# Kernel optimization log

Measured on AMD Instinct MI355X. Metric: run time of the kernel, lower is better.

The kernel has to match this reference:

```python
import jax, jax.numpy as jnp
import numpy as np

L, B, S, D, H, F = 8, 8, 2048, 1024, 16, 4096
DH = D // H
EPS = 1e-5


def setup_inputs() -> dict:
    key = jax.random.key(0)
    ks = jax.random.split(key, 8)
    sc = 0.02
    return {
        "x": jax.random.normal(ks[0], (B, S, D), jnp.float32),
        "layer_indices": jax.random.randint(ks[1], (B,), 0, L, jnp.int32),
        "Wq": jax.random.normal(ks[2], (L, D, D), jnp.float32) * sc,
        "bq": jnp.zeros((L, D), jnp.float32),
        "Wk": jax.random.normal(ks[3], (L, D, D), jnp.float32) * sc,
        "bk": jnp.zeros((L, D), jnp.float32),
        "Wv": jax.random.normal(ks[4], (L, D, D), jnp.float32) * sc,
        "bv": jnp.zeros((L, D), jnp.float32),
        "Wo": jax.random.normal(ks[5], (L, D, D), jnp.float32) * sc,
        "bo": jnp.zeros((L, D), jnp.float32),
        "ln1_s": jnp.ones((L, D), jnp.float32),
        "ln1_b": jnp.zeros((L, D), jnp.float32),
        "ln2_s": jnp.ones((L, D), jnp.float32),
        "ln2_b": jnp.zeros((L, D), jnp.float32),
        "W1": jax.random.normal(ks[6], (L, D, F), jnp.float32) * sc,
        "b1": jnp.zeros((L, F), jnp.float32),
        "W2": jax.random.normal(ks[7], (L, F, D), jnp.float32) * sc,
        "b2": jnp.zeros((L, D), jnp.float32),
    }


def _layernorm(x, s, b):
    # x: [B,S,D]; s,b: [B,D] (per-routed-layer params)
    m = jnp.mean(x, axis=-1, keepdims=True)
    v = jnp.mean(jnp.square(x - m), axis=-1, keepdims=True)
    return (x - m) * jax.lax.rsqrt(v + EPS) * s[:, None, :] + b[:, None, :]


def reference(x, layer_indices, Wq, bq, Wk, bk, Wv, bv, Wo, bo,
              ln1_s, ln1_b, ln2_s, ln2_b, W1, b1, W2, b2):
    idx = layer_indices
    # Gather each batch element's routed layer parameters (MoE-style dispatch).
    Wq_g, bq_g = Wq[idx], bq[idx]
    Wk_g, bk_g = Wk[idx], bk[idx]
    Wv_g, bv_g = Wv[idx], bv[idx]
    Wo_g, bo_g = Wo[idx], bo[idx]
    s1, b1n = ln1_s[idx], ln1_b[idx]
    s2, b2n = ln2_s[idx], ln2_b[idx]
    W1_g, bf1 = W1[idx], b1[idx]
    W2_g, bf2 = W2[idx], b2[idx]

    # --- Multi-head self-attention (pre-LN) ---
    h = _layernorm(x, s1, b1n)                                   # [B,S,D]
    q = jnp.einsum('bsd,bde->bse', h, Wq_g) + bq_g[:, None, :]
    k = jnp.einsum('bsd,bde->bse', h, Wk_g) + bk_g[:, None, :]
    v = jnp.einsum('bsd,bde->bse', h, Wv_g) + bv_g[:, None, :]
    q = q.reshape(B, S, H, DH)
    k = k.reshape(B, S, H, DH)
    v = v.reshape(B, S, H, DH)
    scores = jnp.einsum('bqhd,bkhd->bhqk', q, k) / np.sqrt(DH)   # [B,H,S,S]
    probs = jax.nn.softmax(scores, axis=-1)
    attn = jnp.einsum('bhqk,bkhd->bqhd', probs, v).reshape(B, S, D)
    attn = jnp.einsum('bsd,bde->bse', attn, Wo_g) + bo_g[:, None, :]
    x = x + attn

    # --- Feed-forward (pre-LN) ---
    h = _layernorm(x, s2, b2n)
    h = jax.nn.gelu(jnp.einsum('bsd,bdf->bsf', h, W1_g) + bf1[:, None, :])
    h = jnp.einsum('bsf,bfd->bsd', h, W2_g) + bf2[:, None, :]
    return x + h
```

## Files before the change

### kernel.cpp

```cpp
#include <hip/hip_runtime.h>
#include <cstdint>
#include <cstddef>

typedef __attribute__((ext_vector_type(8))) short s8v;
typedef __attribute__((ext_vector_type(4))) float f4v;

constexpr int Lc = 8, Bc = 8, Sc = 2048, Dc = 1024, Hc = 16, Fc = 4096;

__device__ __forceinline__ unsigned short f2bf(float f) {
    unsigned int u = __float_as_uint(f);
    u = (u + 0x7FFFu + ((u >> 16) & 1u)) >> 16;
    return (unsigned short)u;
}

__global__ __launch_bounds__(256) void transpose_cast(
    const float* __restrict__ in, unsigned short* __restrict__ out, int R, int C) {
    __shared__ float tile[32][33];
    int l = blockIdx.z;
    int r0 = blockIdx.y << 5, c0 = blockIdx.x << 5;
    const float* ip = in + (size_t)l * R * C;
    unsigned short* op = out + (size_t)l * R * C;
    int tx = threadIdx.x & 31, ty = threadIdx.x >> 5;
#pragma unroll
    for (int i = 0; i < 4; i++)
        tile[ty + i * 8][tx] = ip[(size_t)(r0 + ty + i * 8) * C + (c0 + tx)];
    __syncthreads();
#pragma unroll
    for (int i = 0; i < 4; i++)
        op[(size_t)(c0 + ty + i * 8) * R + (r0 + tx)] = f2bf(tile[tx][ty + i * 8]);
}

__global__ __launch_bounds__(256) void ln_kernel(
    const float* __restrict__ x, const float* __restrict__ sc, const float* __restrict__ bi,
    const int* __restrict__ idx, unsigned short* __restrict__ out) {
    int row = blockIdx.x;
    int b = row >> 11;
    int l = idx[b];
    const float* xr = x + (size_t)row * Dc;
    int t = threadIdx.x;
    float4 xv = *(const float4*)(xr + t * 4);
    float s = xv.x + xv.y + xv.z + xv.w;
    float ss = xv.x * xv.x + xv.y * xv.y + xv.z * xv.z + xv.w * xv.w;
#pragma unroll
    for (int off = 32; off; off >>= 1) { s += __shfl_xor(s, off); ss += __shfl_xor(ss, off); }
    __shared__ float red[2][4];
    int w = t >> 6, lane = t & 63;
    if (lane == 0) { red[0][w] = s; red[1][w] = ss; }
    __syncthreads();
    float tot = red[0][0] + red[0][1] + red[0][2] + red[0][3];
    float tots = red[1][0] + red[1][1] + red[1][2] + red[1][3];
    float mean = tot * (1.0f / Dc);
    float var = tots * (1.0f / Dc) - mean * mean;
    float r = rsqrtf(var + 1e-5f);
    float4 s4 = *(const float4*)(sc + (size_t)l * Dc + t * 4);
    float4 b4 = *(const float4*)(bi + (size_t)l * Dc + t * 4);
    ushort4 o;
    o.x = f2bf((xv.x - mean) * r * s4.x + b4.x);
    o.y = f2bf((xv.y - mean) * r * s4.y + b4.y);
    o.z = f2bf((xv.z - mean) * r * s4.z + b4.z);
    o.w = f2bf((xv.w - mean) * r * s4.w + b4.w);
    *(ushort4*)(out + (size_t)row * Dc + t * 4) = o;
}

template <int EPI>
__global__ __launch_bounds__(256) void gemm_kernel(
    const unsigned short* __restrict__ A, const unsigned short* __restrict__ Wt,
    const float* __restrict__ bias, const int* __restrict__ idx,
    const float* __restrict__ resid, void* __restrict__ out, int M, int N, int K) {
    int b = blockIdx.z;
    int l = idx[b];
    int m0 = blockIdx.y << 7, n0 = blockIdx.x << 7;
    const unsigned short* Ab = A + (size_t)b * M * K;
    const unsigned short* Wl = Wt + (size_t)l * N * K;
    __shared__ alignas(16) unsigned short As[128][40];
    __shared__ alignas(16) unsigned short Bs[128][40];
    int tid = threadIdx.x, w = tid >> 6, lane = tid & 63, quad = lane >> 4, lr = lane & 15;
    int wm = (w >> 1) << 6, wn = (w & 1) << 6;
    f4v acc[4][4];
#pragma unroll
    for (int i = 0; i < 4; i++)
#pragma unroll
        for (int j = 0; j < 4; j++) acc[i][j] = 0.f;

    int srow = tid >> 1, soff = (tid & 1) * 16;
    const unsigned short* ag = Ab + (size_t)(m0 + srow) * K + soff;
    const unsigned short* bg = Wl + (size_t)(n0 + srow) * K + soff;

    for (int k0 = 0; k0 < K; k0 += 32) {
        uint4 av0 = *(const uint4*)(ag + k0);
        uint4 av1 = *(const uint4*)(ag + k0 + 8);
        uint4 bv0 = *(const uint4*)(bg + k0);
        uint4 bv1 = *(const uint4*)(bg + k0 + 8);
        __syncthreads();
        *(uint4*)&As[srow][soff] = av0;
        *(uint4*)&As[srow][soff + 8] = av1;
        *(uint4*)&Bs[srow][soff] = bv0;
        *(uint4*)&Bs[srow][soff + 8] = bv1;
        __syncthreads();
        s8v af[4], bf[4];
#pragma unroll
        for (int i = 0; i < 4; i++) af[i] = *(const s8v*)&As[wm + i * 16 + lr][quad * 8];
#pragma unroll
        for (int j = 0; j < 4; j++) bf[j] = *(const s8v*)&Bs[wn + j * 16 + lr][quad * 8];
#pragma unroll
        for (int i = 0; i < 4; i++)
#pragma unroll
            for (int j = 0; j < 4; j++)
                acc[i][j] = __builtin_amdgcn_mfma_f32_16x16x32_bf16(af[i], bf[j], acc[i][j], 0, 0, 0);
    }

    float bj[4];
#pragma unroll
    for (int j = 0; j < 4; j++) bj[j] = bias[(size_t)l * N + (n0 + wn + j * 16 + lr)];
    size_t obase = (size_t)b * M * N;
#pragma unroll
    for (int i = 0; i < 4; i++) {
#pragma unroll
        for (int r = 0; r < 4; r++) {
            int gm = m0 + wm + i * 16 + quad * 4 + r;
            size_t rowoff = obase + (size_t)gm * N;
#pragma unroll
            for (int j = 0; j < 4; j++) {
                int gn = n0 + wn + j * 16 + lr;
                float val = acc[i][j][r] + bj[j];
                if constexpr (EPI == 0) {
                    ((unsigned short*)out)[rowoff + gn] = f2bf(val);
                } else if constexpr (EPI == 1) {
                    float g = 0.5f * val * (1.0f + tanhf(0.7978845608f * (val + 0.044715f * val * val * val)));
                    ((unsigned short*)out)[rowoff + gn] = f2bf(g);
                } else {
                    ((float*)out)[rowoff + gn] = resid[rowoff + gn] + val;
                }
            }
        }
    }
}

__global__ __launch_bounds__(256) void flash_kernel(
    const unsigned short* __restrict__ qm, const unsigned short* __restrict__ km,
    const unsigned short* __restrict__ vm, unsigned short* __restrict__ om) {
    const int b = blockIdx.z, h = blockIdx.y, q0 = blockIdx.x << 6;
    const int tid = threadIdx.x, w = tid >> 6, lane = tid & 63, quad = lane >> 4, lr = lane & 15;
    __shared__ alignas(16) unsigned short Pl[4][16][72];
    __shared__ alignas(16) unsigned short Vt[64][72];
    const size_t bS = (size_t)b * Sc;
    const int hoff = h << 6;

    s8v aq0, aq1;
    {
        const unsigned short* qr = qm + (bS + q0 + w * 16 + lr) * (size_t)Dc + hoff;
        aq0 = *(const s8v*)(qr + quad * 8);
        aq1 = *(const s8v*)(qr + 32 + quad * 8);
    }
    f4v accO[4];
#pragma unroll
    for (int i = 0; i < 4; i++) accO[i] = 0.f;
    float m_i[4] = {-3e38f, -3e38f, -3e38f, -3e38f};
    float l_i[4] = {0.f, 0.f, 0.f, 0.f};

    const int vkey = tid >> 2, vc = tid & 3;

    for (int kv0 = 0; kv0 < Sc; kv0 += 64) {
        const unsigned short* vp = vm + (bS + kv0 + vkey) * (size_t)Dc + hoff + vc * 16;
        s8v v0 = *(const s8v*)vp;
        s8v v1 = *(const s8v*)(vp + 8);
        __syncthreads();
#pragma unroll
        for (int e = 0; e < 8; e++) {
            Vt[vc * 16 + e][vkey] = (unsigned short)v0[e];
            Vt[vc * 16 + 8 + e][vkey] = (unsigned short)v1[e];
        }
        f4v sc4[4];
#pragma unroll
        for (int j = 0; j < 4; j++) {
            const unsigned short* kr = km + (bS + kv0 + j * 16 + lr) * (size_t)Dc + hoff;
            s8v b0 = *(const s8v*)(kr + quad * 8);
            s8v b1 = *(const s8v*)(kr + 32 + quad * 8);
            f4v c = 0.f;
            c = __builtin_amdgcn_mfma_f32_16x16x32_bf16(aq0, b0, c, 0, 0, 0);
            c = __builtin_amdgcn_mfma_f32_16x16x32_bf16(aq1, b1, c, 0, 0, 0);
            sc4[j] = c * 0.125f;
        }
        float alpha[4], pmat[4][4];
#pragma unroll
        for (int rr = 0; rr < 4; rr++) {
            float lm = fmaxf(fmaxf(sc4[0][rr], sc4[1][rr]), fmaxf(sc4[2][rr], sc4[3][rr]));
#pragma unroll
            for (int off = 1; off < 16; off <<= 1) lm = fmaxf(lm, __shfl_xor(lm, off));
            float mn = fmaxf(m_i[rr], lm);
            alpha[rr] = __expf(m_i[rr] - mn);
            m_i[rr] = mn;
            float ls = 0.f;
#pragma unroll
            for (int j = 0; j < 4; j++) {
                float p = __expf(sc4[j][rr] - mn);
                pmat[j][rr] = p;
                ls += p;
            }
#pragma unroll
            for (int off = 1; off < 16; off <<= 1) ls += __shfl_xor(ls, off);
            l_i[rr] = l_i[rr] * alpha[rr] + ls;
        }
#pragma unroll
        for (int jd = 0; jd < 4; jd++)
#pragma unroll
            for (int rr = 0; rr < 4; rr++) accO[jd][rr] *= alpha[rr];
#pragma unroll
        for (int j = 0; j < 4; j++)
#pragma unroll
            for (int rr = 0; rr < 4; rr++)
                Pl[w][quad * 4 + rr][j * 16 + lr] = f2bf(pmat[j][rr]);
        __syncthreads();
        s8v ap0 = *(const s8v*)&Pl[w][lr][quad * 8];
        s8v ap1 = *(const s8v*)&Pl[w][lr][32 + quad * 8];
#pragma unroll
        for (int jd = 0; jd < 4; jd++) {
            s8v b0 = *(const s8v*)&Vt[jd * 16 + lr][quad * 8];
            s8v b1 = *(const s8v*)&Vt[jd * 16 + lr][32 + quad * 8];
            accO[jd] = __builtin_amdgcn_mfma_f32_16x16x32_bf16(ap0, b0, accO[jd], 0, 0, 0);
            accO[jd] = __builtin_amdgcn_mfma_f32_16x16x32_bf16(ap1, b1, accO[jd], 0, 0, 0);
        }
    }
#pragma unroll
    for (int jd = 0; jd < 4; jd++)
#pragma unroll
        for (int rr = 0; rr < 4; rr++)
            om[(bS + q0 + w * 16 + quad * 4 + rr) * (size_t)Dc + hoff + jd * 16 + lr] =
                f2bf(accO[jd][rr] / l_i[rr]);
}

extern "C" void kernel_launch(void* const* d_in, const int* in_sizes, int n_in,
                              void* d_out, int out_size, void* d_ws, size_t ws_size,
                              hipStream_t stream) {
    const float* x  = (const float*)d_in[0];
    const int* idx  = (const int*)d_in[1];
    const float* Wq = (const float*)d_in[2];  const float* bq  = (const float*)d_in[3];
    const float* Wk = (const float*)d_in[4];  const float* bk  = (const float*)d_in[5];
    const float* Wv = (const float*)d_in[6];  const float* bv  = (const float*)d_in[7];
    const float* Wo = (const float*)d_in[8];  const float* bo  = (const float*)d_in[9];
    const float* s1 = (const float*)d_in[10]; const float* b1n = (const float*)d_in[11];
    const float* s2 = (const float*)d_in[12]; const float* b2n = (const float*)d_in[13];
    const float* W1 = (const float*)d_in[14]; const float* bf1 = (const float*)d_in[15];
    const float* W2 = (const float*)d_in[16]; const float* bf2 = (const float*)d_in[17];

    const size_t eDD  = (size_t)Lc * Dc * Dc;
    const size_t eDF  = (size_t)Lc * Dc * Fc;
    const size_t eBSD = (size_t)Bc * Sc * Dc;
    unsigned short* Wtq = (unsigned short*)d_ws;
    unsigned short* Wtk = Wtq + eDD;
    unsigned short* Wtv = Wtk + eDD;
    unsigned short* Wto = Wtv + eDD;
    unsigned short* Wt1 = Wto + eDD;
    unsigned short* Wt2 = Wt1 + eDF;
    unsigned short* hb  = Wt2 + eDF;
    unsigned short* qb  = hb + eBSD;
    unsigned short* kb  = qb + eBSD;
    unsigned short* vb  = kb + eBSD;
    unsigned short* ab  = vb + eBSD;
    float* x2           = (float*)(ab + eBSD);
    unsigned short* fb  = qb;

    dim3 blk(256);
    transpose_cast<<<dim3(Dc / 32, Dc / 32, Lc), blk, 0, stream>>>(Wq, Wtq, Dc, Dc);
    transpose_cast<<<dim3(Dc / 32, Dc / 32, Lc), blk, 0, stream>>>(Wk, Wtk, Dc, Dc);
    transpose_cast<<<dim3(Dc / 32, Dc / 32, Lc), blk, 0, stream>>>(Wv, Wtv, Dc, Dc);
    transpose_cast<<<dim3(Dc / 32, Dc / 32, Lc), blk, 0, stream>>>(Wo, Wto, Dc, Dc);
    transpose_cast<<<dim3(Fc / 32, Dc / 32, Lc), blk, 0, stream>>>(W1, Wt1, Dc, Fc);
    transpose_cast<<<dim3(Dc / 32, Fc / 32, Lc), blk, 0, stream>>>(W2, Wt2, Fc, Dc);
    ln_kernel<<<Bc * Sc, blk, 0, stream>>>(x, s1, b1n, idx, hb);
    gemm_kernel<0><<<dim3(Dc / 128, Sc / 128, Bc), blk, 0, stream>>>(hb, Wtq, bq, idx, nullptr, qb, Sc, Dc, Dc);
    gemm_kernel<0><<<dim3(Dc / 128, Sc / 128, Bc), blk, 0, stream>>>(hb, Wtk, bk, idx, nullptr, kb, Sc, Dc, Dc);
    gemm_kernel<0><<<dim3(Dc / 128, Sc / 128, Bc), blk, 0, stream>>>(hb, Wtv, bv, idx, nullptr, vb, Sc, Dc, Dc);
    flash_kernel<<<dim3(Sc / 64, Hc, Bc), blk, 0, stream>>>(qb, kb, vb, ab);
    gemm_kernel<2><<<dim3(Dc / 128, Sc / 128, Bc), blk, 0, stream>>>(ab, Wto, bo, idx, x, x2, Sc, Dc, Dc);
    ln_kernel<<<Bc * Sc, blk, 0, stream>>>(x2, s2, b2n, idx, hb);
    gemm_kernel<1><<<dim3(Fc / 128, Sc / 128, Bc), blk, 0, stream>>>(hb, Wt1, bf1, idx, nullptr, fb, Sc, Fc, Dc);
    gemm_kernel<2><<<dim3(Dc / 128, Sc / 128, Bc), blk, 0, stream>>>(fb, Wt2, bf2, idx, x2, (float*)d_out, Sc, Dc, Fc);
}
```

Before: 1.845 ms.

## Use direct global-to-LDS loads with swizzle in GEMM and register-only flash attention

The GEMM now stages tiles with global_load_lds into an unpadded LDS layout and applies an XOR swizzle to avoid bank conflicts, which removes the register round-trip. The flash kernel computes S^T so that the probabilities stay in registers as the MFMA B operand, which removes the LDS transposes of P and V. It reads V from a new pre-transposed buffer produced by a separate transpose_v kernel, and it stages the output through LDS so the final stores are coalesced. In exchange there is an extra transpose launch, and flash now reads K and V directly from global memory with no LDS reuse across waves.

After: 2.148 ms. 1.16x slower.

```diff
diff --git a/kernel.cpp b/kernel.cpp
--- a/kernel.cpp
+++ b/kernel.cpp
@@ -11,6 +11,12 @@
     unsigned int u = __float_as_uint(f);
     u = (u + 0x7FFFu + ((u >> 16) & 1u)) >> 16;
     return (unsigned short)u;
+}
+
+__device__ __forceinline__ void gload16(const unsigned short* g, unsigned short* l) {
+    __builtin_amdgcn_global_load_lds(
+        (const __attribute__((address_space(1))) unsigned int*)g,
+        (__attribute__((address_space(3))) unsigned int*)l, 16, 0, 0);
 }
 
 __global__ __launch_bounds__(256) void transpose_cast(
@@ -28,6 +34,23 @@
 #pragma unroll
     for (int i = 0; i < 4; i++)
         op[(size_t)(c0 + ty + i * 8) * R + (r0 + tx)] = f2bf(tile[tx][ty + i * 8]);
+}
+
+__global__ __launch_bounds__(256) void transpose_v(
+    const unsigned short* __restrict__ in, unsigned short* __restrict__ out) {
+    __shared__ unsigned short t[32][33];
+    int bh = blockIdx.z, b = bh >> 4, h = bh & 15;
+    int s0 = blockIdx.x << 5, d0 = blockIdx.y << 5;
+    int tx = threadIdx.x & 31, ty = threadIdx.x >> 5;
+    const unsigned short* ip = in + (size_t)(b * Sc + s0) * Dc + (h << 6) + d0;
+#pragma unroll
+    for (int i = 0; i < 4; i++)
+        t[ty + i * 8][tx] = ip[(size_t)(ty + i * 8) * Dc + tx];
+    __syncthreads();
+    unsigned short* op = out + ((size_t)(b * Hc + h) * 64 + d0) * Sc + s0;
+#pragma unroll
+    for (int i = 0; i < 4; i++)
+        op[(size_t)(ty + i * 8) * Sc + tx] = t[tx][ty + i * 8];
 }
 
 __global__ __launch_bounds__(256) void ln_kernel(
@@ -72,8 +95,8 @@
     int m0 = blockIdx.y << 7, n0 = blockIdx.x << 7;
     const unsigned short* Ab = A + (size_t)b * M * K;
     const unsigned short* Wl = Wt + (size_t)l * N * K;
-    __shared__ alignas(16) unsigned short As[128][40];
-    __shared__ alignas(16) unsigned short Bs[128][40];
+    __shared__ alignas(16) unsigned short As[128 * 32];
+    __shared__ alignas(16) unsigned short Bs[128 * 32];
     int tid = threadIdx.x, w = tid >> 6, lane = tid & 63, quad = lane >> 4, lr = lane & 15;
     int wm = (w >> 1) << 6, wn = (w & 1) << 6;
     f4v acc[4][4];
@@ -82,26 +105,30 @@
 #pragma unroll
         for (int j = 0; j < 4; j++) acc[i][j] = 0.f;
 
-    int srow = tid >> 1, soff = (tid & 1) * 16;
-    const unsigned short* ag = Ab + (size_t)(m0 + srow) * K + soff;
-    const unsigned short* bg = Wl + (size_t)(n0 + srow) * K + soff;
+    int srow = (w << 4) + (lane >> 2);
+    int schunk = (lane & 3) ^ ((lane >> 2) & 3);
+    const unsigned short* ag0 = Ab + (size_t)(m0 + srow) * K + (schunk << 3);
+    const unsigned short* ag1 = Ab + (size_t)(m0 + 64 + srow) * K + (schunk << 3);
+    const unsigned short* bg0 = Wl + (size_t)(n0 + srow) * K + (schunk << 3);
+    const unsigned short* bg1 = Wl + (size_t)(n0 + 64 + srow) * K + (schunk << 3);
+    unsigned short* la0 = As + ((w << 4) << 5);
+    unsigned short* la1 = As + ((64 + (w << 4)) << 5);
+    unsigned short* lb0 = Bs + ((w << 4) << 5);
+    unsigned short* lb1 = Bs + ((64 + (w << 4)) << 5);
+    int fchunk = (quad ^ (lr & 3)) << 3;
 
     for (int k0 = 0; k0 < K; k0 += 32) {
-        uint4 av0 = *(const uint4*)(ag + k0);
-        uint4 av1 = *(const uint4*)(ag + k0 + 8);
-        uint4 bv0 = *(const uint4*)(bg + k0);
-        uint4 bv1 = *(const uint4*)(bg + k0 + 8);
         __syncthreads();
-        *(uint4*)&As[srow][soff] = av0;
-        *(uint4*)&As[srow][soff + 8] = av1;
-        *(uint4*)&Bs[srow][soff] = bv0;
-        *(uint4*)&Bs[srow][soff + 8] = bv1;
+        gload16(ag0 + k0, la0);
+        gload16(ag1 + k0, la1);
+        gload16(bg0 + k0, lb0);
+        gload16(bg1 + k0, lb1);
         __syncthreads();
         s8v af[4], bf[4];
 #pragma unroll
-        for (int i = 0; i < 4; i++) af[i] = *(const s8v*)&As[wm + i * 16 + lr][quad * 8];
-#pragma unroll
-        for (int j = 0; j < 4; j++) bf[j] = *(const s8v*)&Bs[wn + j * 16 + lr][quad * 8];
+        for (int i = 0; i < 4; i++) af[i] = *(const s8v*)&As[((wm + i * 16 + lr) << 5) + fchunk];
+#pragma unroll
+        for (int j = 0; j < 4; j++) bf[j] = *(const s8v*)&Bs[((wn + j * 16 + lr) << 5) + fchunk];
 #pragma unroll
         for (int i = 0; i < 4; i++)
 #pragma unroll
@@ -138,95 +165,94 @@
 
 __global__ __launch_bounds__(256) void flash_kernel(
     const unsigned short* __restrict__ qm, const unsigned short* __restrict__ km,
-    const unsigned short* __restrict__ vm, unsigned short* __restrict__ om) {
+    const unsigned short* __restrict__ vT, unsigned short* __restrict__ om) {
     const int b = blockIdx.z, h = blockIdx.y, q0 = blockIdx.x << 6;
     const int tid = threadIdx.x, w = tid >> 6, lane = tid & 63, quad = lane >> 4, lr = lane & 15;
-    __shared__ alignas(16) unsigned short Pl[4][16][72];
-    __shared__ alignas(16) unsigned short Vt[64][72];
     const size_t bS = (size_t)b * Sc;
     const int hoff = h << 6;
 
-    s8v aq0, aq1;
-    {
-        const unsigned short* qr = qm + (bS + q0 + w * 16 + lr) * (size_t)Dc + hoff;
-        aq0 = *(const s8v*)(qr + quad * 8);
-        aq1 = *(const s8v*)(qr + 32 + quad * 8);
-    }
+    const unsigned short* qr = qm + (bS + q0 + (w << 4) + lr) * (size_t)Dc + hoff + (quad << 3);
+    s8v bq0 = *(const s8v*)qr;
+    s8v bq1 = *(const s8v*)(qr + 32);
+    const int krow_off = ((lr >> 2) << 3) + (lr & 3);
+    const unsigned short* kbase = km + bS * (size_t)Dc + hoff + (quad << 3);
+    const unsigned short* vbase = vT + ((size_t)(b * Hc + h) * 64 + lr) * Sc + (quad << 3);
+
     f4v accO[4];
 #pragma unroll
-    for (int i = 0; i < 4; i++) accO[i] = 0.f;
-    float m_i[4] = {-3e38f, -3e38f, -3e38f, -3e38f};
-    float l_i[4] = {0.f, 0.f, 0.f, 0.f};
-
-    const int vkey = tid >> 2, vc = tid & 3;
+    for (int d = 0; d < 4; d++) accO[d] = 0.f;
+    float m_s = -3e38f, l_s = 0.f;
 
     for (int kv0 = 0; kv0 < Sc; kv0 += 64) {
-        const unsigned short* vp = vm + (bS + kv0 + vkey) * (size_t)Dc + hoff + vc * 16;
-        s8v v0 = *(const s8v*)vp;
-        s8v v1 = *(const s8v*)(vp + 8);
-        __syncthreads();
-#pragma unroll
-        for (int e = 0; e < 8; e++) {
-            Vt[vc * 16 + e][vkey] = (unsigned short)v0[e];
-            Vt[vc * 16 + 8 + e][vkey] = (unsigned short)v1[e];
+        f4v st[4];
+#pragma unroll
+        for (int t = 0; t < 4; t++) {
+            const unsigned short* kr =
+                kbase + (size_t)(kv0 + ((t >> 1) << 5) + ((t & 1) << 2) + krow_off) * Dc;
+            s8v a0 = *(const s8v*)kr;
+            s8v a1 = *(const s8v*)(kr + 32);
+            f4v c;
+            c = 0.f;
+            c = __builtin_amdgcn_mfma_f32_16x16x32_bf16(a0, bq0, c, 0, 0, 0);
+            c = __builtin_amdgcn_mfma_f32_16x16x32_bf16(a1, bq1, c, 0, 0, 0);
+            st[t] = c * 0.125f;
         }
-        f4v sc4[4];
+        float lm = -3e38f;
+#pragma unroll
+        for (int t = 0; t < 4; t++)
+#pragma unroll
+            for (int r = 0; r < 4; r++) lm = fmaxf(lm, st[t][r]);
+        lm = fmaxf(lm, __shfl_xor(lm, 16));
+        lm = fmaxf(lm, __shfl_xor(lm, 32));
+        float mn = fmaxf(m_s, lm);
+        float alpha = __expf(m_s - mn);
+        m_s = mn;
+        float ps[4][4], ls = 0.f;
+#pragma unroll
+        for (int t = 0; t < 4; t++)
+#pragma unroll
+            for (int r = 0; r < 4; r++) { ps[t][r] = __expf(st[t][r] - mn); ls += ps[t][r]; }
+        ls += __shfl_xor(ls, 16);
+        ls += __shfl_xor(ls, 32);
+        l_s = l_s * alpha + ls;
+#pragma unroll
+        for (int d = 0; d < 4; d++) accO[d] *= alpha;
+        s8v pf0, pf1;
 #pragma unroll
         for (int j = 0; j < 4; j++) {
-            const unsigned short* kr = km + (bS + kv0 + j * 16 + lr) * (size_t)Dc + hoff;
-            s8v b0 = *(const s8v*)(kr + quad * 8);
-            s8v b1 = *(const s8v*)(kr + 32 + quad * 8);
-            f4v c = 0.f;
-            c = __builtin_amdgcn_mfma_f32_16x16x32_bf16(aq0, b0, c, 0, 0, 0);
-            c = __builtin_amdgcn_mfma_f32_16x16x32_bf16(aq1, b1, c, 0, 0, 0);
-            sc4[j] = c * 0.125f;
+            pf0[j] = (short)f2bf(ps[0][j]);
+            pf0[4 + j] = (short)f2bf(ps[1][j]);
+            pf1[j] = (short)f2bf(ps[2][j]);
+            pf1[4 + j] = (short)f2bf(ps[3][j]);
         }
-        float alpha[4], pmat[4][4];
-#pragma unroll
-        for (int rr = 0; rr < 4; rr++) {
-            float lm = fmaxf(fmaxf(sc4[0][rr], sc4[1][rr]), fmaxf(sc4[2][rr], sc4[3][rr]));
-#pragma unroll
-            for (int off = 1; off < 16; off <<= 1) lm = fmaxf(lm, __shfl_xor(lm, off));
-            float mn = fmaxf(m_i[rr], lm);
-            alpha[rr] = __expf(m_i[rr] - mn);
-            m_i[rr] = mn;
-            float ls = 0.f;
-#pragma unroll
-            for (int j = 0; j < 4; j++) {
-                float p = __expf(sc4[j][rr] - mn);
-                pmat[j][rr] = p;
-                ls += p;
-            }
-#pragma unroll
-            for (int off = 1; off < 16; off <<= 1) ls += __shfl_xor(ls, off);
-            l_i[rr] = l_i[rr] * alpha[rr] + ls;
-        }
-#pragma unroll
-        for (int jd = 0; jd < 4; jd++)
-#pragma unroll
-            for (int rr = 0; rr < 4; rr++) accO[jd][rr] *= alpha[rr];
-#pragma unroll
-        for (int j = 0; j < 4; j++)
-#pragma unroll
-            for (int rr = 0; rr < 4; rr++)
-                Pl[w][quad * 4 + rr][j * 16 + lr] = f2bf(pmat[j][rr]);
-        __syncthreads();
-        s8v ap0 = *(const s8v*)&Pl[w][lr][quad * 8];
-        s8v ap1 = *(const s8v*)&Pl[w][lr][32 + quad * 8];
-#pragma unroll
-        for (int jd = 0; jd < 4; jd++) {
-            s8v b0 = *(const s8v*)&Vt[jd * 16 + lr][quad * 8];
-            s8v b1 = *(const s8v*)&Vt[jd * 16 + lr][32 + quad * 8];
-            accO[jd] = __builtin_amdgcn_mfma_f32_16x16x32_bf16(ap0, b0, accO[jd], 0, 0, 0);
-            accO[jd] = __builtin_amdgcn_mfma_f32_16x16x32_bf16(ap1, b1, accO[jd], 0, 0, 0);
+#pragma unroll
+        for (int d = 0; d < 4; d++) {
+            const unsigned short* vp = vbase + ((size_t)(d << 4)) * Sc + kv0;
+            s8v v0 = *(const s8v*)vp;
+            s8v v1 = *(const s8v*)(vp + 32);
+            accO[d] = __builtin_amdgcn_mfma_f32_16x16x32_bf16(v0, pf0, accO[d], 0, 0, 0);
+            accO[d] = __builtin_amdgcn_mfma_f32_16x16x32_bf16(v1, pf1, accO[d], 0, 0, 0);
         }
     }
-#pragma unroll
-    for (int jd = 0; jd < 4; jd++)
-#pragma unroll
-        for (int rr = 0; rr < 4; rr++)
-            om[(bS + q0 + w * 16 + quad * 4 + rr) * (size_t)Dc + hoff + jd * 16 + lr] =
-                f2bf(accO[jd][rr] / l_i[rr]);
+
+    __shared__ unsigned short Ot[4][64][17];
+    float inv_l = 1.0f / l_s;
+#pragma unroll
+    for (int d = 0; d < 4; d++)
+#pragma unroll
+        for (int r = 0; r < 4; r++)
+            Ot[w][(d << 4) + (quad << 2) + r][lr] = f2bf(accO[d][r] * inv_l);
+    __syncthreads();
+    int q = lane >> 2, ch = lane & 3;
+    unsigned short* orow = om + (bS + q0 + (w << 4) + q) * (size_t)Dc + hoff + (ch << 4);
+    s8v o0, o1;
+#pragma unroll
+    for (int e = 0; e < 8; e++) {
+        o0[e] = (short)Ot[w][(ch << 4) + e][q];
+        o1[e] = (short)Ot[w][(ch << 4) + 8 + e][q];
+    }
+    *(s8v*)orow = o0;
+    *(s8v*)(orow + 8) = o1;
 }
 
 extern "C" void kernel_launch(void* const* d_in, const int* in_sizes, int n_in,
@@ -259,6 +285,7 @@
     unsigned short* ab  = vb + eBSD;
     float* x2           = (float*)(ab + eBSD);
     unsigned short* fb  = qb;
+    unsigned short* vTb = hb;
 
     dim3 blk(256);
     transpose_cast<<<dim3(Dc / 32, Dc / 32, Lc), blk, 0, stream>>>(Wq, Wtq, Dc, Dc);
@@ -271,7 +298,8 @@
     gemm_kernel<0><<<dim3(Dc / 128, Sc / 128, Bc), blk, 0, stream>>>(hb, Wtq, bq, idx, nullptr, qb, Sc, Dc, Dc);
     gemm_kernel<0><<<dim3(Dc / 128, Sc / 128, Bc), blk, 0, stream>>>(hb, Wtk, bk, idx, nullptr, kb, Sc, Dc, Dc);
     gemm_kernel<0><<<dim3(Dc / 128, Sc / 128, Bc), blk, 0, stream>>>(hb, Wtv, bv, idx, nullptr, vb, Sc, Dc, Dc);
-    flash_kernel<<<dim3(Sc / 64, Hc, Bc), blk, 0, stream>>>(qb, kb, vb, ab);
+    transpose_v<<<dim3(Sc / 32, 2, Bc * Hc), blk, 0, stream>>>(vb, vTb);
+    flash_kernel<<<dim3(Sc / 64, Hc, Bc), blk, 0, stream>>>(qb, kb, vTb, ab);
     gemm_kernel<2><<<dim3(Dc / 128, Sc / 128, Bc), blk, 0, stream>>>(ab, Wto, bo, idx, x, x2, Sc, Dc, Dc);
     ln_kernel<<<Bc * Sc, blk, 0, stream>>>(x2, s2, b2n, idx, hb);
     gemm_kernel<1><<<dim3(Fc / 128, Sc / 128, Bc), blk, 0, stream>>>(hb, Wt1, bf1, idx, nullptr, fb, Sc, Fc, Dc);
```
